# Kernel tuning notes

Hardware: AMD Instinct MI355X
Metric: run time of the kernel (lower is better)

The kernel has to match this reference:

```python
import jax, jax.numpy as jnp
import numpy as np

NUM_NODES = 100000
NUM_EDGES = 50000
N_INC = 1000000  # incidence pairs (node, hyperedge)
IN_DIM = 128
EDGE_DIM = 128
NODE_DIM = 128


def _glorot(key, fan_in, fan_out):
    lim = float(np.sqrt(6.0 / (fan_in + fan_out)))
    return jax.random.uniform(key, (fan_in, fan_out), jnp.float32, -lim, lim)


def _prelu(x, a):
    return jnp.where(x >= 0, x, a * x)


def setup_inputs() -> dict:
    key = jax.random.key(0)
    ks = jax.random.split(key, 7)
    x = jax.random.normal(ks[0], (NUM_NODES, IN_DIM), jnp.float32)
    node_idx = jax.random.randint(ks[1], (N_INC,), 0, NUM_NODES, jnp.int32)
    edge_idx = jax.random.randint(ks[2], (N_INC,), 0, NUM_EDGES, jnp.int32)
    hyperedge_index = jnp.stack([node_idx, edge_idx])  # [2, N_INC]
    return dict(
        x=x,
        hyperedge_index=hyperedge_index,
        W_n2e_0=_glorot(ks[3], IN_DIM, EDGE_DIM),
        W_e2n_0=_glorot(ks[4], EDGE_DIM, NODE_DIM),
        bias_0=jnp.zeros((NODE_DIM,), jnp.float32),
        W_n2e_1=_glorot(ks[5], NODE_DIM, EDGE_DIM),
        W_e2n_1=_glorot(ks[6], EDGE_DIM, NODE_DIM),
        bias_1=jnp.zeros((NODE_DIM,), jnp.float32),
        alpha=jnp.float32(0.25),  # shared nn.PReLU() parameter
        num_nodes=NUM_NODES,
        num_edges=NUM_EDGES,
    )


def _conv(x, node_idx, edge_idx, Dn_inv, De_inv, W_n2e, W_e2n, b, alpha,
          num_nodes, num_edges):
    # node -> hyperedge: row-normalized scatter-add (norm = De^{-1} per target edge)
    xe = x @ W_n2e                                              # [N, E_dim]
    msg_e = xe[node_idx] * De_inv[edge_idx][:, None]            # [N_INC, E_dim]
    e = jax.ops.segment_sum(msg_e, edge_idx, num_segments=num_edges)
    e = _prelu(e, alpha)
    # hyperedge -> node: norm = Dn^{-1} per target node
    xn = e @ W_e2n                                              # [M, D]
    msg_n = xn[edge_idx] * Dn_inv[node_idx][:, None]            # [N_INC, D]
    n = jax.ops.segment_sum(msg_n, node_idx, num_segments=num_nodes) + b
    return n, e


def reference(x, hyperedge_index, W_n2e_0, W_e2n_0, bias_0, W_n2e_1, W_e2n_1,
              bias_1, alpha, num_nodes, num_edges):
    node_idx = hyperedge_index[0]
    edge_idx = hyperedge_index[1]
    ones = jnp.ones((node_idx.shape[0],), jnp.float32)
    Dn = jax.ops.segment_sum(ones, node_idx, num_segments=num_nodes)
    De = jax.ops.segment_sum(ones, edge_idx, num_segments=num_edges)
    Dn_inv = jnp.where(Dn > 0, 1.0 / jnp.where(Dn > 0, Dn, 1.0), 0.0)
    De_inv = jnp.where(De > 0, 1.0 / jnp.where(De > 0, De, 1.0), 0.0)

    n, e = _conv(x, node_idx, edge_idx, Dn_inv, De_inv,
                 W_n2e_0, W_e2n_0, bias_0, alpha, num_nodes, num_edges)
    n = _prelu(n, alpha)  # encoder-level activation between layers
    n, e = _conv(n, node_idx, edge_idx, Dn_inv, De_inv,
                 W_n2e_1, W_e2n_1, bias_1, alpha, num_nodes, num_edges)
    n = _prelu(n, alpha)
    return n, e
```

## Files before the change

### kernel.cpp

```cpp
#include <hip/hip_runtime.h>
#include <stdint.h>

#define NN 100000
#define NE 50000
#define NBLK 256
#define NBK 196
#define ESH 8
#define NSH 9

using bf16x8 = __attribute__((ext_vector_type(8))) short;
using f32x4  = __attribute__((ext_vector_type(4))) float;

__device__ inline unsigned f2bf(float f) {
  union { float f; unsigned u; } x; x.f = f;
  unsigned u = x.u;
  return (u + 0x7FFFu + ((u >> 16) & 1u)) >> 16;
}
__device__ inline float bfbits2f(unsigned bits) {
  union { unsigned u; float f; } x; x.u = bits;
  return x.f;
}


__global__ __launch_bounds__(256) void hist_kernel(const int* __restrict__ nidx,
                                                   const int* __restrict__ eidx, int ni,
                                                   int* __restrict__ He, int* __restrict__ Hn) {
  __shared__ int he[NBK], hn[NBK];
  for (int t = threadIdx.x; t < NBK; t += 256) { he[t] = 0; hn[t] = 0; }
  __syncthreads();
  int chunk = (ni + NBLK - 1) / NBLK;
  int s = blockIdx.x * chunk, e = min(s + chunk, ni);
  for (int i = s + threadIdx.x; i < e; i += 256) {
    atomicAdd(&he[eidx[i] >> ESH], 1);
    atomicAdd(&hn[nidx[i] >> NSH], 1);
  }
  __syncthreads();
  for (int t = threadIdx.x; t < NBK; t += 256) {
    He[t * NBLK + blockIdx.x] = he[t];
    Hn[t * NBLK + blockIdx.x] = hn[t];
  }
}

__global__ __launch_bounds__(256) void scanH_kernel(int* __restrict__ He, int* __restrict__ Hn,
                                                    int* __restrict__ ebb, int* __restrict__ nbb,
                                                    int ni) {
  int* H = blockIdx.x ? Hn : He;
  int* bb = blockIdx.x ? nbb : ebb;
  __shared__ int tot[256];
  int t = threadIdx.x;
  int sum = 0;
  if (t < NBK)
    for (int b = 0; b < NBLK; b++) sum += H[t * NBLK + b];
  tot[t] = sum;
  __syncthreads();
  for (int o = 1; o < 256; o <<= 1) {
    int v = (t >= o) ? tot[t - o] : 0;
    __syncthreads();
    tot[t] += v;
    __syncthreads();
  }
  int base = (t > 0) ? tot[t - 1] : 0;
  if (t < NBK) {
    bb[t] = base;
    int run = base;
    for (int b = 0; b < NBLK; b++) {
      int old = H[t * NBLK + b];
      H[t * NBLK + b] = run;
      run += old;
    }
  }
  if (t == 0) bb[NBK] = ni;
}

__global__ __launch_bounds__(256) void scatter_kernel(const int* __restrict__ nidx,
                                                      const int* __restrict__ eidx, int ni,
                                                      const int* __restrict__ He,
                                                      const int* __restrict__ Hn,
                                                      int2* __restrict__ binE,
                                                      int2* __restrict__ binN) {
  __shared__ int ce[NBK], cn[NBK];
  for (int t = threadIdx.x; t < NBK; t += 256) {
    ce[t] = He[t * NBLK + blockIdx.x];
    cn[t] = Hn[t * NBLK + blockIdx.x];
  }
  __syncthreads();
  int chunk = (ni + NBLK - 1) / NBLK;
  int s = blockIdx.x * chunk, e = min(s + chunk, ni);
  for (int i = s + threadIdx.x; i < e; i += 256) {
    int nd = nidx[i], ed = eidx[i];
    int pe = atomicAdd(&ce[ed >> ESH], 1);
    binE[pe] = make_int2(nd, ed);
    int pn = atomicAdd(&cn[nd >> NSH], 1);
    binN[pn] = make_int2(ed, nd);
  }
}

__global__ __launch_bounds__(256) void finalize_kernel(const int2* __restrict__ binE,
                                                       const int2* __restrict__ binN,
                                                       const int* __restrict__ ebb,
                                                       const int* __restrict__ nbb,
                                                       int* __restrict__ eoff, int* __restrict__ noff,
                                                       float* __restrict__ einv, float* __restrict__ ninv,
                                                       int* __restrict__ edge_nodes,
                                                       int* __restrict__ node_edges, int ni) {
  __shared__ int cnt[512], excl[512], sc[256];
  bool isE = blockIdx.x < NBK;
  int b = isE ? blockIdx.x : blockIdx.x - NBK;
  const int2* bin = isE ? binE : binN;
  const int* bb = isE ? ebb : nbb;
  int* off = isE ? eoff : noff;
  float* inv = isE ? einv : ninv;
  int* out = isE ? edge_nodes : node_edges;
  int NT = isE ? NE : NN;
  int sh = isE ? ESH : NSH;
  int tbase = b << sh;
  int nt = min(1 << sh, NT - tbase);
  int t = threadIdx.x;
  cnt[t] = 0; cnt[t + 256] = 0;
  __syncthreads();
  int s = bb[b], e = bb[b + 1];
  for (int i = s + t; i < e; i += 256) atomicAdd(&cnt[bin[i].y - tbase], 1);
  __syncthreads();
  int p = cnt[2 * t] + cnt[2 * t + 1];
  sc[t] = p;
  __syncthreads();
  for (int o = 1; o < 256; o <<= 1) {
    int v = (t >= o) ? sc[t - o] : 0;
    __syncthreads();
    sc[t] += v;
    __syncthreads();
  }
  int pb = (t > 0) ? sc[t - 1] : 0;
  excl[2 * t] = pb;
  excl[2 * t + 1] = pb + cnt[2 * t];
  __syncthreads();
  for (int lt = t; lt < nt; lt += 256) {
    off[tbase + lt] = s + excl[lt];
    int c = cnt[lt];
    inv[tbase + lt] = (c > 0) ? 1.0f / (float)c : 0.0f;
  }
  if (b == NBK - 1 && t == 0) off[NT] = ni;
  __syncthreads();
  cnt[t] = 0; cnt[t + 256] = 0;
  __syncthreads();
  for (int i = s + t; i < e; i += 256) {
    int2 it = bin[i];
    int lt = it.y - tbase;
    int pos = s + excl[lt] + atomicAdd(&cnt[lt], 1);
    out[pos] = it.x;
  }
}

__global__ void packw_kernel(const float* __restrict__ w0, const float* __restrict__ w1,
                             const float* __restrict__ w2, const float* __restrict__ w3,
                             short* __restrict__ wp) {
  int gid = blockIdx.x * blockDim.x + threadIdx.x;
  if (gid >= 4 * 16384) return;
  int w = gid >> 14, r = gid & 16383;
  int j = r & 7, lane = (r >> 3) & 63, kk = (r >> 9) & 3, ct = (r >> 11) & 7;
  int k = kk * 32 + (lane >> 4) * 8 + j;
  int c = ct * 16 + (lane & 15);
  const float* W = (w == 0) ? w0 : (w == 1) ? w1 : (w == 2) ? w2 : w3;
  wp[gid] = (short)f2bf(W[k * 128 + c]);
}

__global__ __launch_bounds__(256) void cvtrow_kernel(const float* __restrict__ x,
                                                     uint4* __restrict__ xb) {
  size_t q = (size_t)blockIdx.x * 256 + threadIdx.x;
  const float4* xf = (const float4*)x;
  float4 lo = xf[q * 2], hi = xf[q * 2 + 1];
  uint4 o;
  o.x = (f2bf(lo.x) & 0xffffu) | (f2bf(lo.y) << 16);
  o.y = (f2bf(lo.z) & 0xffffu) | (f2bf(lo.w) << 16);
  o.z = (f2bf(hi.x) & 0xffffu) | (f2bf(hi.y) << 16);
  o.w = (f2bf(hi.z) & 0xffffu) | (f2bf(hi.w) << 16);
  xb[q] = o;
}

template <bool PRELU, int OMODE>
__global__ __launch_bounds__(256) void gemm_kernel(const short* __restrict__ Ap,
                                                   const short* __restrict__ Wp,
                                                   short* __restrict__ Cb,
                                                   float* __restrict__ Cf,
                                                   const float* __restrict__ alpha_p, int M) {
  int wave = threadIdx.x >> 6;
  int lane = threadIdx.x & 63;
  int rt = blockIdx.x * 4 + wave;
  if (rt * 16 >= M) return;
  int kg = lane >> 4;
  int rloc = lane & 15;
  int row = rt * 16 + rloc;
  const short* arow = Ap + (size_t)row * 128 + kg * 8;
  bf16x8 a[4];
#pragma unroll
  for (int kk = 0; kk < 4; kk++) a[kk] = *(const bf16x8*)(arow + kk * 32);
  float al = PRELU ? *alpha_p : 0.f;
#pragma unroll
  for (int ct = 0; ct < 8; ct++) {
    f32x4 acc = {0.f, 0.f, 0.f, 0.f};
#pragma unroll
    for (int kk = 0; kk < 4; kk++) {
      bf16x8 bfr = *(const bf16x8*)(Wp + ((size_t)(ct * 4 + kk) * 64 + lane) * 8);
      acc = __builtin_amdgcn_mfma_f32_16x16x32_bf16(a[kk], bfr, acc, 0, 0, 0);
    }
    int col = ct * 16 + rloc;
#pragma unroll
    for (int j = 0; j < 4; j++) {
      int rj = rt * 16 + kg * 4 + j;
      float v = acc[j];
      if constexpr (PRELU) v = (v >= 0.f) ? v : al * v;
      if constexpr (OMODE == 0) {
        Cb[(size_t)rj * 128 + col] = (short)f2bf(v);
      } else {
        Cf[(size_t)rj * 128 + col] = v;
        Cb[(size_t)rj * 128 + col] = (short)f2bf(v);
      }
    }
  }
}

template <bool PRELU, bool OBF>
__global__ __launch_bounds__(256) void gather_kernel(const uint4* __restrict__ src,
                                                     void* __restrict__ dst,
                                                     const int* __restrict__ off,
                                                     const int* __restrict__ ids,
                                                     const float* __restrict__ inv,
                                                     const float* __restrict__ bias,
                                                     const float* __restrict__ alpha_p, int T) {
  int tgt = blockIdx.x * 16 + (threadIdx.x >> 4);
  if (tgt >= T) return;
  int c = threadIdx.x & 15;
  int s = off[tgt], e = off[tgt + 1];
  float r[8] = {0, 0, 0, 0, 0, 0, 0, 0};
  int i = s;
  for (; i + 8 <= e; i += 8) {
    int idv[8];
#pragma unroll
    for (int u = 0; u < 8; u++) idv[u] = ids[i + u];
    uint4 v[8];
#pragma unroll
    for (int u = 0; u < 8; u++) v[u] = src[(size_t)idv[u] * 16 + c];
#pragma unroll
    for (int u = 0; u < 8; u++) {
      r[0] += bfbits2f(v[u].x << 16); r[1] += bfbits2f(v[u].x & 0xffff0000u);
      r[2] += bfbits2f(v[u].y << 16); r[3] += bfbits2f(v[u].y & 0xffff0000u);
      r[4] += bfbits2f(v[u].z << 16); r[5] += bfbits2f(v[u].z & 0xffff0000u);
      r[6] += bfbits2f(v[u].w << 16); r[7] += bfbits2f(v[u].w & 0xffff0000u);
    }
  }
  for (; i < e; i++) {
    uint4 v = src[(size_t)ids[i] * 16 + c];
    r[0] += bfbits2f(v.x << 16); r[1] += bfbits2f(v.x & 0xffff0000u);
    r[2] += bfbits2f(v.y << 16); r[3] += bfbits2f(v.y & 0xffff0000u);
    r[4] += bfbits2f(v.z << 16); r[5] += bfbits2f(v.z & 0xffff0000u);
    r[6] += bfbits2f(v.w << 16); r[7] += bfbits2f(v.w & 0xffff0000u);
  }
  float scv = inv[tgt];
  float al = PRELU ? *alpha_p : 0.f;
  float b[8] = {0, 0, 0, 0, 0, 0, 0, 0};
  if (bias) {
    float4 b0 = ((const float4*)bias)[c * 2];
    float4 b1 = ((const float4*)bias)[c * 2 + 1];
    b[0] = b0.x; b[1] = b0.y; b[2] = b0.z; b[3] = b0.w;
    b[4] = b1.x; b[5] = b1.y; b[6] = b1.z; b[7] = b1.w;
  }
#pragma unroll
  for (int j = 0; j < 8; j++) {
    float v = r[j] * scv + b[j];
    if constexpr (PRELU) v = (v >= 0.f) ? v : al * v;
    r[j] = v;
  }
  if constexpr (OBF) {
    uint4 o;
    o.x = (f2bf(r[0]) & 0xffffu) | (f2bf(r[1]) << 16);
    o.y = (f2bf(r[2]) & 0xffffu) | (f2bf(r[3]) << 16);
    o.z = (f2bf(r[4]) & 0xffffu) | (f2bf(r[5]) << 16);
    o.w = (f2bf(r[6]) & 0xffffu) | (f2bf(r[7]) << 16);
    ((uint4*)dst)[(size_t)tgt * 16 + c] = o;
  } else {
    float4 o0; o0.x = r[0]; o0.y = r[1]; o0.z = r[2]; o0.w = r[3];
    float4 o1; o1.x = r[4]; o1.y = r[5]; o1.z = r[6]; o1.w = r[7];
    ((float4*)dst)[(size_t)tgt * 32 + c * 2] = o0;
    ((float4*)dst)[(size_t)tgt * 32 + c * 2 + 1] = o1;
  }
}

extern "C" void kernel_launch(void* const* d_in, const int* in_sizes, int n_in,
                              void* d_out, int out_size, void* d_ws, size_t ws_size,
                              hipStream_t stream) {
  const float* x = (const float*)d_in[0];
  const int* nidx = (const int*)d_in[1];
  int NI = in_sizes[1] / 2;
  const int* eidx = nidx + NI;
  const float* W0 = (const float*)d_in[2];
  const float* W1 = (const float*)d_in[3];
  const float* b0 = (const float*)d_in[4];
  const float* W2 = (const float*)d_in[5];
  const float* W3 = (const float*)d_in[6];
  const float* b1 = (const float*)d_in[7];
  const float* alpha = (const float*)d_in[8];

  char* ws = (char*)d_ws;
  size_t o = 0;
  auto alloc = [&](size_t bytes) { void* p = ws + o; o += (bytes + 255) & ~255ull; return p; };
  int* He = (int*)alloc((size_t)NBK * NBLK * 4);
  int* Hn = (int*)alloc((size_t)NBK * NBLK * 4);
  int* ebb = (int*)alloc((NBK + 1) * 4);
  int* nbb = (int*)alloc((NBK + 1) * 4);
  int* eoff = (int*)alloc((size_t)(NE + 1) * 4);
  int* noff = (int*)alloc((size_t)(NN + 1) * 4);
  float* einv = (float*)alloc((size_t)NE * 4);
  float* ninv = (float*)alloc((size_t)NN * 4);
  int* edge_nodes = (int*)alloc((size_t)NI * 4);
  int* node_edges = (int*)alloc((size_t)NI * 4);
  short* wp = (short*)alloc((size_t)4 * 16384 * 2);
  char* arena = (char*)alloc((size_t)NN * 128 * 2 + (size_t)NE * 128 * 2 * 3);
  int2* binE = (int2*)arena;
  int2* binN = (int2*)(arena + (size_t)NI * 8);
  short* xb = (short*)arena;
  short* Ge = (short*)(arena + (size_t)NN * 128 * 2);
  short* eb = (short*)(arena + (size_t)NN * 128 * 2 + (size_t)NE * 128 * 2);
  short* xn = (short*)(arena + (size_t)NN * 128 * 2 + (size_t)NE * 128 * 2 * 2);

  float* outN = (float*)d_out;
  float* outE = outN + (size_t)NN * 128;

  hist_kernel<<<NBLK, 256, 0, stream>>>(nidx, eidx, NI, He, Hn);
  scanH_kernel<<<2, 256, 0, stream>>>(He, Hn, ebb, nbb, NI);
  scatter_kernel<<<NBLK, 256, 0, stream>>>(nidx, eidx, NI, He, Hn, binE, binN);
  finalize_kernel<<<2 * NBK, 256, 0, stream>>>(binE, binN, ebb, nbb, eoff, noff,
                                               einv, ninv, edge_nodes, node_edges, NI);
  packw_kernel<<<256, 256, 0, stream>>>(W0, W1, W2, W3, wp);
  cvtrow_kernel<<<NN * 128 / 8 / 256, 256, 0, stream>>>(x, (uint4*)xb);

  int gE = ((NE / 16) + 3) / 4;
  int ggE = NE / 16;
  int ggN = (NN + 15) / 16;

  gather_kernel<false, true><<<ggE, 256, 0, stream>>>((const uint4*)xb, Ge, eoff, edge_nodes,
                                                      einv, nullptr, alpha, NE);
  gemm_kernel<true, 0><<<gE, 256, 0, stream>>>(Ge, wp + 0 * 16384, eb, nullptr, alpha, NE);
  gemm_kernel<false, 0><<<gE, 256, 0, stream>>>(eb, wp + 1 * 16384, xn, nullptr, alpha, NE);
  short* n1 = xb;
  gather_kernel<true, true><<<ggN, 256, 0, stream>>>((const uint4*)xn, n1, noff, node_edges,
                                                     ninv, b0, alpha, NN);
  gather_kernel<false, true><<<ggE, 256, 0, stream>>>((const uint4*)n1, Ge, eoff, edge_nodes,
                                                      einv, nullptr, alpha, NE);
  gemm_kernel<true, 2><<<gE, 256, 0, stream>>>(Ge, wp + 2 * 16384, eb, outE, alpha, NE);
  gemm_kernel<false, 0><<<gE, 256, 0, stream>>>(eb, wp + 3 * 16384, xn, nullptr, alpha, NE);
  gather_kernel<true, false><<<ggN, 256, 0, stream>>>((const uint4*)xn, outN, noff, node_edges,
                                                      ninv, b1, alpha, NN);
}
```

Baseline: 299.4 us.

## Fuse edge gather with both edge-side GEMMs through an LDS tile

```diff
diff --git a/kernel.cpp b/kernel.cpp
--- a/kernel.cpp
+++ b/kernel.cpp
@@ -177,49 +177,118 @@
   xb[q] = o;
 }
 
-template <bool PRELU, int OMODE>
-__global__ __launch_bounds__(256) void gemm_kernel(const short* __restrict__ Ap,
-                                                   const short* __restrict__ Wp,
-                                                   short* __restrict__ Cb,
-                                                   float* __restrict__ Cf,
-                                                   const float* __restrict__ alpha_p, int M) {
+template <bool WEF32>
+__global__ __launch_bounds__(256) void fusedE_kernel(const uint4* __restrict__ src,
+                                                     const short* __restrict__ wpA,
+                                                     const short* __restrict__ wpB,
+                                                     const int* __restrict__ off,
+                                                     const int* __restrict__ ids,
+                                                     const float* __restrict__ inv,
+                                                     const float* __restrict__ alpha_p,
+                                                     short* __restrict__ xn,
+                                                     float* __restrict__ eoutf, int M) {
+  __shared__ short tile[64][136];
   int wave = threadIdx.x >> 6;
   int lane = threadIdx.x & 63;
-  int rt = blockIdx.x * 4 + wave;
-  if (rt * 16 >= M) return;
+  int gl = lane >> 4;
+  int c = lane & 15;
+  int base = blockIdx.x * 64;
+
+  for (int q = 0; q < 4; q++) {
+    int lrow = wave * 16 + gl * 4 + q;
+    int tgt = base + lrow;
+    if (tgt >= M) break;
+    int s = off[tgt], e = off[tgt + 1];
+    float r[8] = {0, 0, 0, 0, 0, 0, 0, 0};
+    int i = s;
+    for (; i + 8 <= e; i += 8) {
+      int idv[8];
+#pragma unroll
+      for (int u = 0; u < 8; u++) idv[u] = ids[i + u];
+      uint4 v[8];
+#pragma unroll
+      for (int u = 0; u < 8; u++) v[u] = src[(size_t)idv[u] * 16 + c];
+#pragma unroll
+      for (int u = 0; u < 8; u++) {
+        r[0] += bfbits2f(v[u].x << 16); r[1] += bfbits2f(v[u].x & 0xffff0000u);
+        r[2] += bfbits2f(v[u].y << 16); r[3] += bfbits2f(v[u].y & 0xffff0000u);
+        r[4] += bfbits2f(v[u].z << 16); r[5] += bfbits2f(v[u].z & 0xffff0000u);
+        r[6] += bfbits2f(v[u].w << 16); r[7] += bfbits2f(v[u].w & 0xffff0000u);
+      }
+    }
+    for (; i < e; i++) {
+      uint4 v = src[(size_t)ids[i] * 16 + c];
+      r[0] += bfbits2f(v.x << 16); r[1] += bfbits2f(v.x & 0xffff0000u);
+      r[2] += bfbits2f(v.y << 16); r[3] += bfbits2f(v.y & 0xffff0000u);
+      r[4] += bfbits2f(v.z << 16); r[5] += bfbits2f(v.z & 0xffff0000u);
+      r[6] += bfbits2f(v.w << 16); r[7] += bfbits2f(v.w & 0xffff0000u);
+    }
+    float scv = inv[tgt];
+    uint4 o;
+    o.x = (f2bf(r[0] * scv) & 0xffffu) | (f2bf(r[1] * scv) << 16);
+    o.y = (f2bf(r[2] * scv) & 0xffffu) | (f2bf(r[3] * scv) << 16);
+    o.z = (f2bf(r[4] * scv) & 0xffffu) | (f2bf(r[5] * scv) << 16);
+    o.w = (f2bf(r[6] * scv) & 0xffffu) | (f2bf(r[7] * scv) << 16);
+    *(uint4*)&tile[lrow][c * 8] = o;
+  }
+
   int kg = lane >> 4;
   int rloc = lane & 15;
-  int row = rt * 16 + rloc;
-  const short* arow = Ap + (size_t)row * 128 + kg * 8;
+  float al = *alpha_p;
   bf16x8 a[4];
 #pragma unroll
-  for (int kk = 0; kk < 4; kk++) a[kk] = *(const bf16x8*)(arow + kk * 32);
-  float al = PRELU ? *alpha_p : 0.f;
+  for (int kk = 0; kk < 4; kk++)
+    a[kk] = *(const bf16x8*)&tile[wave * 16 + rloc][kg * 8 + kk * 32];
+  f32x4 acc1[8];
 #pragma unroll
   for (int ct = 0; ct < 8; ct++) {
     f32x4 acc = {0.f, 0.f, 0.f, 0.f};
 #pragma unroll
     for (int kk = 0; kk < 4; kk++) {
-      bf16x8 bfr = *(const bf16x8*)(Wp + ((size_t)(ct * 4 + kk) * 64 + lane) * 8);
+      bf16x8 bfr = *(const bf16x8*)(wpA + ((size_t)(ct * 4 + kk) * 64 + lane) * 8);
       acc = __builtin_amdgcn_mfma_f32_16x16x32_bf16(a[kk], bfr, acc, 0, 0, 0);
     }
+#pragma unroll
+    for (int j = 0; j < 4; j++) {
+      float v = acc[j];
+      acc[j] = (v >= 0.f) ? v : al * v;
+    }
+    acc1[ct] = acc;
+  }
+#pragma unroll
+  for (int ct = 0; ct < 8; ct++) {
     int col = ct * 16 + rloc;
 #pragma unroll
     for (int j = 0; j < 4; j++) {
-      int rj = rt * 16 + kg * 4 + j;
-      float v = acc[j];
-      if constexpr (PRELU) v = (v >= 0.f) ? v : al * v;
-      if constexpr (OMODE == 0) {
-        Cb[(size_t)rj * 128 + col] = (short)f2bf(v);
-      } else {
-        Cf[(size_t)rj * 128 + col] = v;
-        Cb[(size_t)rj * 128 + col] = (short)f2bf(v);
-      }
-    }
-  }
-}
-
-template <bool PRELU, bool OBF>
+      int lrow = wave * 16 + kg * 4 + j;
+      int grow = base + lrow;
+      if (WEF32 && grow < M) eoutf[(size_t)grow * 128 + col] = acc1[ct][j];
+      tile[lrow][col] = (short)f2bf(acc1[ct][j]);
+    }
+  }
+
+  bf16x8 a2[4];
+#pragma unroll
+  for (int kk = 0; kk < 4; kk++)
+    a2[kk] = *(const bf16x8*)&tile[wave * 16 + rloc][kg * 8 + kk * 32];
+#pragma unroll
+  for (int ct = 0; ct < 8; ct++) {
+    f32x4 acc = {0.f, 0.f, 0.f, 0.f};
+#pragma unroll
+    for (int kk = 0; kk < 4; kk++) {
+      bf16x8 bfr = *(const bf16x8*)(wpB + ((size_t)(ct * 4 + kk) * 64 + lane) * 8);
+      acc = __builtin_amdgcn_mfma_f32_16x16x32_bf16(a2[kk], bfr, acc, 0, 0, 0);
+    }
+    int col = ct * 16 + rloc;
+#pragma unroll
+    for (int j = 0; j < 4; j++) {
+      int grow = base + wave * 16 + kg * 4 + j;
+      if (grow < M) xn[(size_t)grow * 128 + col] = (short)f2bf(acc[j]);
+    }
+  }
+}
+
+template <bool OBF>
 __global__ __launch_bounds__(256) void gather_kernel(const uint4* __restrict__ src,
                                                      void* __restrict__ dst,
                                                      const int* __restrict__ off,
@@ -256,9 +325,9 @@
     r[6] += bfbits2f(v.w << 16); r[7] += bfbits2f(v.w & 0xffff0000u);
   }
   float scv = inv[tgt];
-  float al = PRELU ? *alpha_p : 0.f;
-  float b[8] = {0, 0, 0, 0, 0, 0, 0, 0};
-  if (bias) {
+  float al = *alpha_p;
+  float b[8];
+  {
     float4 b0 = ((const float4*)bias)[c * 2];
     float4 b1 = ((const float4*)bias)[c * 2 + 1];
     b[0] = b0.x; b[1] = b0.y; b[2] = b0.z; b[3] = b0.w;
@@ -267,8 +336,7 @@
 #pragma unroll
   for (int j = 0; j < 8; j++) {
     float v = r[j] * scv + b[j];
-    if constexpr (PRELU) v = (v >= 0.f) ? v : al * v;
-    r[j] = v;
+    r[j] = (v >= 0.f) ? v : al * v;
   }
   if constexpr (OBF) {
     uint4 o;
@@ -314,13 +382,11 @@
   int* edge_nodes = (int*)alloc((size_t)NI * 4);
   int* node_edges = (int*)alloc((size_t)NI * 4);
   short* wp = (short*)alloc((size_t)4 * 16384 * 2);
-  char* arena = (char*)alloc((size_t)NN * 128 * 2 + (size_t)NE * 128 * 2 * 3);
+  char* arena = (char*)alloc((size_t)NN * 128 * 2 + (size_t)NE * 128 * 2);
   int2* binE = (int2*)arena;
   int2* binN = (int2*)(arena + (size_t)NI * 8);
   short* xb = (short*)arena;
-  short* Ge = (short*)(arena + (size_t)NN * 128 * 2);
-  short* eb = (short*)(arena + (size_t)NN * 128 * 2 + (size_t)NE * 128 * 2);
-  short* xn = (short*)(arena + (size_t)NN * 128 * 2 + (size_t)NE * 128 * 2 * 2);
+  short* xn = (short*)(arena + (size_t)NN * 128 * 2);
 
   float* outN = (float*)d_out;
   float* outE = outN + (size_t)NN * 128;
@@ -333,21 +399,18 @@
   packw_kernel<<<256, 256, 0, stream>>>(W0, W1, W2, W3, wp);
   cvtrow_kernel<<<NN * 128 / 8 / 256, 256, 0, stream>>>(x, (uint4*)xb);
 
-  int gE = ((NE / 16) + 3) / 4;
-  int ggE = NE / 16;
+  int gfE = (NE + 63) / 64;
   int ggN = (NN + 15) / 16;
 
-  gather_kernel<false, true><<<ggE, 256, 0, stream>>>((const uint4*)xb, Ge, eoff, edge_nodes,
-                                                      einv, nullptr, alpha, NE);
-  gemm_kernel<true, 0><<<gE, 256, 0, stream>>>(Ge, wp + 0 * 16384, eb, nullptr, alpha, NE);
-  gemm_kernel<false, 0><<<gE, 256, 0, stream>>>(eb, wp + 1 * 16384, xn, nullptr, alpha, NE);
+  fusedE_kernel<false><<<gfE, 256, 0, stream>>>((const uint4*)xb, wp + 0 * 16384,
+                                                wp + 1 * 16384, eoff, edge_nodes, einv,
+                                                alpha, xn, nullptr, NE);
   short* n1 = xb;
-  gather_kernel<true, true><<<ggN, 256, 0, stream>>>((const uint4*)xn, n1, noff, node_edges,
-                                                     ninv, b0, alpha, NN);
-  gather_kernel<false, true><<<ggE, 256, 0, stream>>>((const uint4*)n1, Ge, eoff, edge_nodes,
-                                                      einv, nullptr, alpha, NE);
-  gemm_kernel<true, 2><<<gE, 256, 0, stream>>>(Ge, wp + 2 * 16384, eb, outE, alpha, NE);
-  gemm_kernel<false, 0><<<gE, 256, 0, stream>>>(eb, wp + 3 * 16384, xn, nullptr, alpha, NE);
-  gather_kernel<true, false><<<ggN, 256, 0, stream>>>((const uint4*)xn, outN, noff, node_edges,
-                                                      ninv, b1, alpha, NN);
-}
+  gather_kernel<true><<<ggN, 256, 0, stream>>>((const uint4*)xn, n1, noff, node_edges,
+                                               ninv, b0, alpha, NN);
+  fusedE_kernel<true><<<gfE, 256, 0, stream>>>((const uint4*)n1, wp + 2 * 16384,
+                                               wp + 3 * 16384, eoff, edge_nodes, einv,
+                                               alpha, xn, outE, NE);
+  gather_kernel<false><<<ggN, 256, 0, stream>>>((const uint4*)xn, outN, noff, node_edges,
+                                                ninv, b1, alpha, NN);
+}
```

Result: no change. 299.6 us (+0.1%).

## Split feature rows into half-planes for gathers and fuse back-to-back GEMMs via LDS

Applied to the files above, without the earlier changes.

```diff
diff --git a/kernel.cpp b/kernel.cpp
--- a/kernel.cpp
+++ b/kernel.cpp
@@ -164,9 +164,12 @@
   wp[gid] = (short)f2bf(W[k * 128 + c]);
 }
 
-__global__ __launch_bounds__(256) void cvtrow_kernel(const float* __restrict__ x,
-                                                     uint4* __restrict__ xb) {
+__global__ __launch_bounds__(256) void cvtsplit_kernel(const float* __restrict__ x,
+                                                       uint4* __restrict__ xb) {
   size_t q = (size_t)blockIdx.x * 256 + threadIdx.x;
+  size_t row = q >> 4;
+  int seg = (int)(q & 15);
+  int plane = seg >> 3, within = seg & 7;
   const float4* xf = (const float4*)x;
   float4 lo = xf[q * 2], hi = xf[q * 2 + 1];
   uint4 o;
@@ -174,63 +177,23 @@
   o.y = (f2bf(lo.z) & 0xffffu) | (f2bf(lo.w) << 16);
   o.z = (f2bf(hi.x) & 0xffffu) | (f2bf(hi.y) << 16);
   o.w = (f2bf(hi.z) & 0xffffu) | (f2bf(hi.w) << 16);
-  xb[q] = o;
-}
-
-template <bool PRELU, int OMODE>
-__global__ __launch_bounds__(256) void gemm_kernel(const short* __restrict__ Ap,
-                                                   const short* __restrict__ Wp,
-                                                   short* __restrict__ Cb,
-                                                   float* __restrict__ Cf,
-                                                   const float* __restrict__ alpha_p, int M) {
-  int wave = threadIdx.x >> 6;
-  int lane = threadIdx.x & 63;
-  int rt = blockIdx.x * 4 + wave;
-  if (rt * 16 >= M) return;
-  int kg = lane >> 4;
-  int rloc = lane & 15;
-  int row = rt * 16 + rloc;
-  const short* arow = Ap + (size_t)row * 128 + kg * 8;
-  bf16x8 a[4];
-#pragma unroll
-  for (int kk = 0; kk < 4; kk++) a[kk] = *(const bf16x8*)(arow + kk * 32);
-  float al = PRELU ? *alpha_p : 0.f;
-#pragma unroll
-  for (int ct = 0; ct < 8; ct++) {
-    f32x4 acc = {0.f, 0.f, 0.f, 0.f};
-#pragma unroll
-    for (int kk = 0; kk < 4; kk++) {
-      bf16x8 bfr = *(const bf16x8*)(Wp + ((size_t)(ct * 4 + kk) * 64 + lane) * 8);
-      acc = __builtin_amdgcn_mfma_f32_16x16x32_bf16(a[kk], bfr, acc, 0, 0, 0);
-    }
-    int col = ct * 16 + rloc;
-#pragma unroll
-    for (int j = 0; j < 4; j++) {
-      int rj = rt * 16 + kg * 4 + j;
-      float v = acc[j];
-      if constexpr (PRELU) v = (v >= 0.f) ? v : al * v;
-      if constexpr (OMODE == 0) {
-        Cb[(size_t)rj * 128 + col] = (short)f2bf(v);
-      } else {
-        Cf[(size_t)rj * 128 + col] = v;
-        Cb[(size_t)rj * 128 + col] = (short)f2bf(v);
-      }
-    }
-  }
+  xb[((size_t)plane * NN + row) * 8 + within] = o;
 }
 
 template <bool PRELU, bool OBF>
-__global__ __launch_bounds__(256) void gather_kernel(const uint4* __restrict__ src,
-                                                     void* __restrict__ dst,
-                                                     const int* __restrict__ off,
-                                                     const int* __restrict__ ids,
-                                                     const float* __restrict__ inv,
-                                                     const float* __restrict__ bias,
-                                                     const float* __restrict__ alpha_p, int T) {
-  int tgt = blockIdx.x * 16 + (threadIdx.x >> 4);
+__global__ __launch_bounds__(256) void gatherh_kernel(const uint4* __restrict__ src,
+                                                      void* __restrict__ dst,
+                                                      const int* __restrict__ off,
+                                                      const int* __restrict__ ids,
+                                                      const float* __restrict__ inv,
+                                                      const float* __restrict__ bias,
+                                                      const float* __restrict__ alpha_p,
+                                                      int T, int Rsrc, int h) {
+  int tgt = blockIdx.x * 32 + (threadIdx.x >> 3);
   if (tgt >= T) return;
-  int c = threadIdx.x & 15;
+  int c = threadIdx.x & 7;
   int s = off[tgt], e = off[tgt + 1];
+  const uint4* base = src + (size_t)h * Rsrc * 8 + c;
   float r[8] = {0, 0, 0, 0, 0, 0, 0, 0};
   int i = s;
   for (; i + 8 <= e; i += 8) {
@@ -239,7 +202,7 @@
     for (int u = 0; u < 8; u++) idv[u] = ids[i + u];
     uint4 v[8];
 #pragma unroll
-    for (int u = 0; u < 8; u++) v[u] = src[(size_t)idv[u] * 16 + c];
+    for (int u = 0; u < 8; u++) v[u] = base[(size_t)idv[u] * 8];
 #pragma unroll
     for (int u = 0; u < 8; u++) {
       r[0] += bfbits2f(v[u].x << 16); r[1] += bfbits2f(v[u].x & 0xffff0000u);
@@ -249,7 +212,7 @@
     }
   }
   for (; i < e; i++) {
-    uint4 v = src[(size_t)ids[i] * 16 + c];
+    uint4 v = base[(size_t)ids[i] * 8];
     r[0] += bfbits2f(v.x << 16); r[1] += bfbits2f(v.x & 0xffff0000u);
     r[2] += bfbits2f(v.y << 16); r[3] += bfbits2f(v.y & 0xffff0000u);
     r[4] += bfbits2f(v.z << 16); r[5] += bfbits2f(v.z & 0xffff0000u);
@@ -259,8 +222,8 @@
   float al = PRELU ? *alpha_p : 0.f;
   float b[8] = {0, 0, 0, 0, 0, 0, 0, 0};
   if (bias) {
-    float4 b0 = ((const float4*)bias)[c * 2];
-    float4 b1 = ((const float4*)bias)[c * 2 + 1];
+    float4 b0 = ((const float4*)bias)[h * 16 + c * 2];
+    float4 b1 = ((const float4*)bias)[h * 16 + c * 2 + 1];
     b[0] = b0.x; b[1] = b0.y; b[2] = b0.z; b[3] = b0.w;
     b[4] = b1.x; b[5] = b1.y; b[6] = b1.z; b[7] = b1.w;
   }
@@ -276,12 +239,83 @@
     o.y = (f2bf(r[2]) & 0xffffu) | (f2bf(r[3]) << 16);
     o.z = (f2bf(r[4]) & 0xffffu) | (f2bf(r[5]) << 16);
     o.w = (f2bf(r[6]) & 0xffffu) | (f2bf(r[7]) << 16);
-    ((uint4*)dst)[(size_t)tgt * 16 + c] = o;
+    ((uint4*)dst)[((size_t)h * T + tgt) * 8 + c] = o;
   } else {
     float4 o0; o0.x = r[0]; o0.y = r[1]; o0.z = r[2]; o0.w = r[3];
     float4 o1; o1.x = r[4]; o1.y = r[5]; o1.z = r[6]; o1.w = r[7];
-    ((float4*)dst)[(size_t)tgt * 32 + c * 2] = o0;
-    ((float4*)dst)[(size_t)tgt * 32 + c * 2 + 1] = o1;
+    ((float4*)dst)[(size_t)tgt * 32 + h * 16 + c * 2] = o0;
+    ((float4*)dst)[(size_t)tgt * 32 + h * 16 + c * 2 + 1] = o1;
+  }
+}
+
+template <bool WEF32>
+__global__ __launch_bounds__(256) void gemm12_kernel(const short* __restrict__ A,
+                                                     const short* __restrict__ wpA,
+                                                     const short* __restrict__ wpB,
+                                                     const float* __restrict__ alpha_p,
+                                                     short* __restrict__ xn,
+                                                     float* __restrict__ eoutf, int M) {
+  __shared__ short tile[64][136];
+  int wave = threadIdx.x >> 6;
+  int lane = threadIdx.x & 63;
+  int kg = lane >> 4;
+  int rloc = lane & 15;
+  int base = blockIdx.x * 64;
+  int row = base + wave * 16 + rloc;
+  float al = *alpha_p;
+
+  bf16x8 a[4];
+  if (row < M) {
+    const short* p0 = A + (size_t)row * 64 + kg * 8;
+    const short* p1 = A + ((size_t)M + row) * 64 + kg * 8;
+    a[0] = *(const bf16x8*)p0;
+    a[1] = *(const bf16x8*)(p0 + 32);
+    a[2] = *(const bf16x8*)p1;
+    a[3] = *(const bf16x8*)(p1 + 32);
+  } else {
+#pragma unroll
+    for (int kk = 0; kk < 4; kk++) a[kk] = bf16x8{0, 0, 0, 0, 0, 0, 0, 0};
+  }
+
+#pragma unroll
+  for (int ct = 0; ct < 8; ct++) {
+    f32x4 acc = {0.f, 0.f, 0.f, 0.f};
+#pragma unroll
+    for (int kk = 0; kk < 4; kk++) {
+      bf16x8 bfr = *(const bf16x8*)(wpA + ((size_t)(ct * 4 + kk) * 64 + lane) * 8);
+      acc = __builtin_amdgcn_mfma_f32_16x16x32_bf16(a[kk], bfr, acc, 0, 0, 0);
+    }
+    int col = ct * 16 + rloc;
+#pragma unroll
+    for (int j = 0; j < 4; j++) {
+      float v = acc[j];
+      v = (v >= 0.f) ? v : al * v;
+      int lrow = wave * 16 + kg * 4 + j;
+      int grow = base + lrow;
+      if (WEF32 && grow < M) eoutf[(size_t)grow * 128 + col] = v;
+      tile[lrow][col] = (short)f2bf(v);
+    }
+  }
+
+  bf16x8 a2[4];
+#pragma unroll
+  for (int kk = 0; kk < 4; kk++)
+    a2[kk] = *(const bf16x8*)&tile[wave * 16 + rloc][kg * 8 + kk * 32];
+#pragma unroll
+  for (int ct = 0; ct < 8; ct++) {
+    f32x4 acc = {0.f, 0.f, 0.f, 0.f};
+#pragma unroll
+    for (int kk = 0; kk < 4; kk++) {
+      bf16x8 bfr = *(const bf16x8*)(wpB + ((size_t)(ct * 4 + kk) * 64 + lane) * 8);
+      acc = __builtin_amdgcn_mfma_f32_16x16x32_bf16(a2[kk], bfr, acc, 0, 0, 0);
+    }
+    int plane = ct >> 2;
+    int colh = (ct & 3) * 16 + rloc;
+#pragma unroll
+    for (int j = 0; j < 4; j++) {
+      int grow = base + wave * 16 + kg * 4 + j;
+      if (grow < M) xn[((size_t)plane * M + grow) * 64 + colh] = (short)f2bf(acc[j]);
+    }
   }
 }
 
@@ -314,13 +348,12 @@
   int* edge_nodes = (int*)alloc((size_t)NI * 4);
   int* node_edges = (int*)alloc((size_t)NI * 4);
   short* wp = (short*)alloc((size_t)4 * 16384 * 2);
-  char* arena = (char*)alloc((size_t)NN * 128 * 2 + (size_t)NE * 128 * 2 * 3);
+  char* arena = (char*)alloc((size_t)NN * 128 * 2 + (size_t)NE * 128 * 2 * 2);
   int2* binE = (int2*)arena;
   int2* binN = (int2*)(arena + (size_t)NI * 8);
   short* xb = (short*)arena;
   short* Ge = (short*)(arena + (size_t)NN * 128 * 2);
-  short* eb = (short*)(arena + (size_t)NN * 128 * 2 + (size_t)NE * 128 * 2);
-  short* xn = (short*)(arena + (size_t)NN * 128 * 2 + (size_t)NE * 128 * 2 * 2);
+  short* xn = (short*)(arena + (size_t)NN * 128 * 2 + (size_t)NE * 128 * 2);
 
   float* outN = (float*)d_out;
   float* outE = outN + (size_t)NN * 128;
@@ -331,23 +364,31 @@
   finalize_kernel<<<2 * NBK, 256, 0, stream>>>(binE, binN, ebb, nbb, eoff, noff,
                                                einv, ninv, edge_nodes, node_edges, NI);
   packw_kernel<<<256, 256, 0, stream>>>(W0, W1, W2, W3, wp);
-  cvtrow_kernel<<<NN * 128 / 8 / 256, 256, 0, stream>>>(x, (uint4*)xb);
-
-  int gE = ((NE / 16) + 3) / 4;
-  int ggE = NE / 16;
-  int ggN = (NN + 15) / 16;
-
-  gather_kernel<false, true><<<ggE, 256, 0, stream>>>((const uint4*)xb, Ge, eoff, edge_nodes,
-                                                      einv, nullptr, alpha, NE);
-  gemm_kernel<true, 0><<<gE, 256, 0, stream>>>(Ge, wp + 0 * 16384, eb, nullptr, alpha, NE);
-  gemm_kernel<false, 0><<<gE, 256, 0, stream>>>(eb, wp + 1 * 16384, xn, nullptr, alpha, NE);
+  cvtsplit_kernel<<<NN * 128 / 8 / 256, 256, 0, stream>>>(x, (uint4*)xb);
+
+  int ggE = (NE + 31) / 32;
+  int ggN = (NN + 31) / 32;
+  int gfE = (NE + 63) / 64;
+
+  gatherh_kernel<false, true><<<ggE, 256, 0, stream>>>((const uint4*)xb, Ge, eoff, edge_nodes,
+                                                       einv, nullptr, alpha, NE, NN, 0);
+  gatherh_kernel<false, true><<<ggE, 256, 0, stream>>>((const uint4*)xb, Ge, eoff, edge_nodes,
+                                                       einv, nullptr, alpha, NE, NN, 1);
+  gemm12_kernel<false><<<gfE, 256, 0, stream>>>(Ge, wp + 0 * 16384, wp + 1 * 16384,
+                                                alpha, xn, nullptr, NE);
   short* n1 = xb;
-  gather_kernel<true, true><<<ggN, 256, 0, stream>>>((const uint4*)xn, n1, noff, node_edges,
-                                                     ninv, b0, alpha, NN);
-  gather_kernel<false, true><<<ggE, 256, 0, stream>>>((const uint4*)n1, Ge, eoff, edge_nodes,
-                                                      einv, nullptr, alpha, NE);
-  gemm_kernel<true, 2><<<gE, 256, 0, stream>>>(Ge, wp + 2 * 16384, eb, outE, alpha, NE);
-  gemm_kernel<false, 0><<<gE, 256, 0, stream>>>(eb, wp + 3 * 16384, xn, nullptr, alpha, NE);
-  gather_kernel<true, false><<<ggN, 256, 0, stream>>>((const uint4*)xn, outN, noff, node_edges,
-                                                      ninv, b1, alpha, NN);
-}
+  gatherh_kernel<true, true><<<ggN, 256, 0, stream>>>((const uint4*)xn, n1, noff, node_edges,
+                                                      ninv, b0, alpha, NN, NE, 0);
+  gatherh_kernel<true, true><<<ggN, 256, 0, stream>>>((const uint4*)xn, n1, noff, node_edges,
+                                                      ninv, b0, alpha, NN, NE, 1);
+  gatherh_kernel<false, true><<<ggE, 256, 0, stream>>>((const uint4*)n1, Ge, eoff, edge_nodes,
+                                                       einv, nullptr, alpha, NE, NN, 0);
+  gatherh_kernel<false, true><<<ggE, 256, 0, stream>>>((const uint4*)n1, Ge, eoff, edge_nodes,
+                                                       einv, nullptr, alpha, NE, NN, 1);
+  gemm12_kernel<true><<<gfE, 256, 0, stream>>>(Ge, wp + 2 * 16384, wp + 3 * 16384,
+                                               alpha, xn, outE, NE);
+  gatherh_kernel<true, false><<<ggN, 256, 0, stream>>>((const uint4*)xn, outN, noff, node_edges,
+                                                       ninv, b1, alpha, NN, NE, 0);
+  gatherh_kernel<true, false><<<ggN, 256, 0, stream>>>((const uint4*)xn, outN, noff, node_edges,
+                                                       ninv, b1, alpha, NN, NE, 1);
+}
```

After: 317.4 us. +6.0%, slower.

## Fuse back-to-back edge GEMMs via LDS tile and pack bin entries to 32 bits

Applied to the files above, without the earlier changes.

```diff
diff --git a/kernel.cpp b/kernel.cpp
--- a/kernel.cpp
+++ b/kernel.cpp
@@ -76,8 +76,8 @@
                                                       const int* __restrict__ eidx, int ni,
                                                       const int* __restrict__ He,
                                                       const int* __restrict__ Hn,
-                                                      int2* __restrict__ binE,
-                                                      int2* __restrict__ binN) {
+                                                      unsigned* __restrict__ binE,
+                                                      unsigned* __restrict__ binN) {
   __shared__ int ce[NBK], cn[NBK];
   for (int t = threadIdx.x; t < NBK; t += 256) {
     ce[t] = He[t * NBLK + blockIdx.x];
@@ -89,14 +89,14 @@
   for (int i = s + threadIdx.x; i < e; i += 256) {
     int nd = nidx[i], ed = eidx[i];
     int pe = atomicAdd(&ce[ed >> ESH], 1);
-    binE[pe] = make_int2(nd, ed);
+    binE[pe] = (unsigned)nd | ((unsigned)(ed & 255) << 17);
     int pn = atomicAdd(&cn[nd >> NSH], 1);
-    binN[pn] = make_int2(ed, nd);
-  }
-}
-
-__global__ __launch_bounds__(256) void finalize_kernel(const int2* __restrict__ binE,
-                                                       const int2* __restrict__ binN,
+    binN[pn] = (unsigned)ed | ((unsigned)(nd & 511) << 16);
+  }
+}
+
+__global__ __launch_bounds__(256) void finalize_kernel(const unsigned* __restrict__ binE,
+                                                       const unsigned* __restrict__ binN,
                                                        const int* __restrict__ ebb,
                                                        const int* __restrict__ nbb,
                                                        int* __restrict__ eoff, int* __restrict__ noff,
@@ -106,20 +106,22 @@
   __shared__ int cnt[512], excl[512], sc[256];
   bool isE = blockIdx.x < NBK;
   int b = isE ? blockIdx.x : blockIdx.x - NBK;
-  const int2* bin = isE ? binE : binN;
+  const unsigned* bin = isE ? binE : binN;
   const int* bb = isE ? ebb : nbb;
   int* off = isE ? eoff : noff;
   float* inv = isE ? einv : ninv;
   int* out = isE ? edge_nodes : node_edges;
   int NT = isE ? NE : NN;
   int sh = isE ? ESH : NSH;
+  int psh = isE ? 17 : 16;
+  unsigned smask = (1u << psh) - 1u;
   int tbase = b << sh;
   int nt = min(1 << sh, NT - tbase);
   int t = threadIdx.x;
   cnt[t] = 0; cnt[t + 256] = 0;
   __syncthreads();
   int s = bb[b], e = bb[b + 1];
-  for (int i = s + t; i < e; i += 256) atomicAdd(&cnt[bin[i].y - tbase], 1);
+  for (int i = s + t; i < e; i += 256) atomicAdd(&cnt[bin[i] >> psh], 1);
   __syncthreads();
   int p = cnt[2 * t] + cnt[2 * t + 1];
   sc[t] = p;
@@ -144,10 +146,10 @@
   cnt[t] = 0; cnt[t + 256] = 0;
   __syncthreads();
   for (int i = s + t; i < e; i += 256) {
-    int2 it = bin[i];
-    int lt = it.y - tbase;
+    unsigned it = bin[i];
+    int lt = it >> psh;
     int pos = s + excl[lt] + atomicAdd(&cnt[lt], 1);
-    out[pos] = it.x;
+    out[pos] = (int)(it & smask);
   }
 }
 
@@ -175,48 +177,6 @@
   o.z = (f2bf(hi.x) & 0xffffu) | (f2bf(hi.y) << 16);
   o.w = (f2bf(hi.z) & 0xffffu) | (f2bf(hi.w) << 16);
   xb[q] = o;
-}
-
-template <bool PRELU, int OMODE>
-__global__ __launch_bounds__(256) void gemm_kernel(const short* __restrict__ Ap,
-                                                   const short* __restrict__ Wp,
-                                                   short* __restrict__ Cb,
-                                                   float* __restrict__ Cf,
-                                                   const float* __restrict__ alpha_p, int M) {
-  int wave = threadIdx.x >> 6;
-  int lane = threadIdx.x & 63;
-  int rt = blockIdx.x * 4 + wave;
-  if (rt * 16 >= M) return;
-  int kg = lane >> 4;
-  int rloc = lane & 15;
-  int row = rt * 16 + rloc;
-  const short* arow = Ap + (size_t)row * 128 + kg * 8;
-  bf16x8 a[4];
-#pragma unroll
-  for (int kk = 0; kk < 4; kk++) a[kk] = *(const bf16x8*)(arow + kk * 32);
-  float al = PRELU ? *alpha_p : 0.f;
-#pragma unroll
-  for (int ct = 0; ct < 8; ct++) {
-    f32x4 acc = {0.f, 0.f, 0.f, 0.f};
-#pragma unroll
-    for (int kk = 0; kk < 4; kk++) {
-      bf16x8 bfr = *(const bf16x8*)(Wp + ((size_t)(ct * 4 + kk) * 64 + lane) * 8);
-      acc = __builtin_amdgcn_mfma_f32_16x16x32_bf16(a[kk], bfr, acc, 0, 0, 0);
-    }
-    int col = ct * 16 + rloc;
-#pragma unroll
-    for (int j = 0; j < 4; j++) {
-      int rj = rt * 16 + kg * 4 + j;
-      float v = acc[j];
-      if constexpr (PRELU) v = (v >= 0.f) ? v : al * v;
-      if constexpr (OMODE == 0) {
-        Cb[(size_t)rj * 128 + col] = (short)f2bf(v);
-      } else {
-        Cf[(size_t)rj * 128 + col] = v;
-        Cb[(size_t)rj * 128 + col] = (short)f2bf(v);
-      }
-    }
-  }
 }
 
 template <bool PRELU, bool OBF>
@@ -285,6 +245,73 @@
   }
 }
 
+template <bool WEF32>
+__global__ __launch_bounds__(256) void gemm12_kernel(const short* __restrict__ A,
+                                                     const short* __restrict__ wpA,
+                                                     const short* __restrict__ wpB,
+                                                     const float* __restrict__ alpha_p,
+                                                     short* __restrict__ xn,
+                                                     float* __restrict__ eoutf, int M) {
+  __shared__ short tile[64][136];
+  int wave = threadIdx.x >> 6;
+  int lane = threadIdx.x & 63;
+  int kg = lane >> 4;
+  int rloc = lane & 15;
+  int base = blockIdx.x * 64;
+  int row = base + wave * 16 + rloc;
+  float al = *alpha_p;
+
+  bf16x8 a[4];
+  if (row < M) {
+    const short* arow = A + (size_t)row * 128 + kg * 8;
+#pragma unroll
+    for (int kk = 0; kk < 4; kk++) a[kk] = *(const bf16x8*)(arow + kk * 32);
+  } else {
+#pragma unroll
+    for (int kk = 0; kk < 4; kk++) a[kk] = bf16x8{0, 0, 0, 0, 0, 0, 0, 0};
+  }
+
+#pragma unroll
+  for (int ct = 0; ct < 8; ct++) {
+    f32x4 acc = {0.f, 0.f, 0.f, 0.f};
+#pragma unroll
+    for (int kk = 0; kk < 4; kk++) {
+      bf16x8 bfr = *(const bf16x8*)(wpA + ((size_t)(ct * 4 + kk) * 64 + lane) * 8);
+      acc = __builtin_amdgcn_mfma_f32_16x16x32_bf16(a[kk], bfr, acc, 0, 0, 0);
+    }
+    int col = ct * 16 + rloc;
+#pragma unroll
+    for (int j = 0; j < 4; j++) {
+      float v = acc[j];
+      v = (v >= 0.f) ? v : al * v;
+      int lrow = wave * 16 + kg * 4 + j;
+      int grow = base + lrow;
+      if (WEF32 && grow < M) eoutf[(size_t)grow * 128 + col] = v;
+      tile[lrow][col] = (short)f2bf(v);
+    }
+  }
+
+  bf16x8 a2[4];
+#pragma unroll
+  for (int kk = 0; kk < 4; kk++)
+    a2[kk] = *(const bf16x8*)&tile[wave * 16 + rloc][kg * 8 + kk * 32];
+#pragma unroll
+  for (int ct = 0; ct < 8; ct++) {
+    f32x4 acc = {0.f, 0.f, 0.f, 0.f};
+#pragma unroll
+    for (int kk = 0; kk < 4; kk++) {
+      bf16x8 bfr = *(const bf16x8*)(wpB + ((size_t)(ct * 4 + kk) * 64 + lane) * 8);
+      acc = __builtin_amdgcn_mfma_f32_16x16x32_bf16(a2[kk], bfr, acc, 0, 0, 0);
+    }
+    int col = ct * 16 + rloc;
+#pragma unroll
+    for (int j = 0; j < 4; j++) {
+      int grow = base + wave * 16 + kg * 4 + j;
+      if (grow < M) xn[(size_t)grow * 128 + col] = (short)f2bf(acc[j]);
+    }
+  }
+}
+
 extern "C" void kernel_launch(void* const* d_in, const int* in_sizes, int n_in,
                               void* d_out, int out_size, void* d_ws, size_t ws_size,
                               hipStream_t stream) {
@@ -314,13 +341,12 @@
   int* edge_nodes = (int*)alloc((size_t)NI * 4);
   int* node_edges = (int*)alloc((size_t)NI * 4);
   short* wp = (short*)alloc((size_t)4 * 16384 * 2);
-  char* arena = (char*)alloc((size_t)NN * 128 * 2 + (size_t)NE * 128 * 2 * 3);
-  int2* binE = (int2*)arena;
-  int2* binN = (int2*)(arena + (size_t)NI * 8);
+  char* arena = (char*)alloc((size_t)NN * 128 * 2 + (size_t)NE * 128 * 2 * 2);
+  unsigned* binE = (unsigned*)arena;
+  unsigned* binN = (unsigned*)(arena + (size_t)NI * 4);
   short* xb = (short*)arena;
   short* Ge = (short*)(arena + (size_t)NN * 128 * 2);
-  short* eb = (short*)(arena + (size_t)NN * 128 * 2 + (size_t)NE * 128 * 2);
-  short* xn = (short*)(arena + (size_t)NN * 128 * 2 + (size_t)NE * 128 * 2 * 2);
+  short* xn = (short*)(arena + (size_t)NN * 128 * 2 + (size_t)NE * 128 * 2);
 
   float* outN = (float*)d_out;
   float* outE = outN + (size_t)NN * 128;
@@ -333,21 +359,21 @@
   packw_kernel<<<256, 256, 0, stream>>>(W0, W1, W2, W3, wp);
   cvtrow_kernel<<<NN * 128 / 8 / 256, 256, 0, stream>>>(x, (uint4*)xb);
 
-  int gE = ((NE / 16) + 3) / 4;
+  int gfE = (NE + 63) / 64;
   int ggE = NE / 16;
   int ggN = (NN + 15) / 16;
 
   gather_kernel<false, true><<<ggE, 256, 0, stream>>>((const uint4*)xb, Ge, eoff, edge_nodes,
                                                       einv, nullptr, alpha, NE);
-  gemm_kernel<true, 0><<<gE, 256, 0, stream>>>(Ge, wp + 0 * 16384, eb, nullptr, alpha, NE);
-  gemm_kernel<false, 0><<<gE, 256, 0, stream>>>(eb, wp + 1 * 16384, xn, nullptr, alpha, NE);
+  gemm12_kernel<false><<<gfE, 256, 0, stream>>>(Ge, wp + 0 * 16384, wp + 1 * 16384,
+                                                alpha, xn, nullptr, NE);
   short* n1 = xb;
   gather_kernel<true, true><<<ggN, 256, 0, stream>>>((const uint4*)xn, n1, noff, node_edges,
                                                      ninv, b0, alpha, NN);
   gather_kernel<false, true><<<ggE, 256, 0, stream>>>((const uint4*)n1, Ge, eoff, edge_nodes,
                                                       einv, nullptr, alpha, NE);
-  gemm_kernel<true, 2><<<gE, 256, 0, stream>>>(Ge, wp + 2 * 16384, eb, outE, alpha, NE);
-  gemm_kernel<false, 0><<<gE, 256, 0, stream>>>(eb, wp + 3 * 16384, xn, nullptr, alpha, NE);
+  gemm12_kernel<true><<<gfE, 256, 0, stream>>>(Ge, wp + 2 * 16384, wp + 3 * 16384,
+                                               alpha, xn, outE, NE);
   gather_kernel<true, false><<<ggN, 256, 0, stream>>>((const uint4*)xn, outN, noff, node_edges,
                                                       ninv, b1, alpha, NN);
 }
```

Measured after the change: 288.2 us (median of 2 runs). 3.7% less time.
